# Optimization experiments

Measured on AMD Instinct MI355X. Metric: run time of the kernel, lower is better.

The kernel has to match this reference:

```python
import jax, jax.numpy as jnp
import numpy as np

T, B, IN, H1, H2, H3 = 128, 256, 512, 1024, 1024, 512


def _glorot(key, shape, fan):
    bound = 1.0 / np.sqrt(fan)
    return jax.random.uniform(key, shape, jnp.float32, -bound, bound)


def _cell_params(key, in_dim, h_dim):
    k = jax.random.split(key, 4)
    return (_glorot(k[0], (4 * h_dim, in_dim), h_dim),
            _glorot(k[1], (4 * h_dim, h_dim), h_dim),
            _glorot(k[2], (4 * h_dim,), h_dim),
            _glorot(k[3], (4 * h_dim,), h_dim))


def setup_inputs() -> dict:
    key = jax.random.key(0)
    ks = jax.random.split(key, 4)
    x = jax.random.normal(ks[0], (T, B, IN), jnp.float32)
    Wih1, Whh1, bih1, bhh1 = _cell_params(ks[1], IN, H1)
    Wih2, Whh2, bih2, bhh2 = _cell_params(ks[2], H1, H2)
    Wih3, Whh3, bih3, bhh3 = _cell_params(ks[3], H2, H3)
    return dict(input_seq=x,
                Wih1=Wih1, Whh1=Whh1, bih1=bih1, bhh1=bhh1,
                Wih2=Wih2, Whh2=Whh2, bih2=bih2, bhh2=bhh2,
                Wih3=Wih3, Whh3=Whh3, bih3=bih3, bhh3=bhh3)


def _lstm_cell(x, h, c, Wih, Whh, bih, bhh):
    # PyTorch LSTMCell gate order: i, f, g, o
    gates = x @ Wih.T + bih + h @ Whh.T + bhh
    i, f, g, o = jnp.split(gates, 4, axis=-1)
    c_new = jax.nn.sigmoid(f) * c + jax.nn.sigmoid(i) * jnp.tanh(g)
    h_new = jax.nn.sigmoid(o) * jnp.tanh(c_new)
    return h_new, c_new


def reference(input_seq, Wih1, Whh1, bih1, bhh1,
              Wih2, Whh2, bih2, bhh2,
              Wih3, Whh3, bih3, bhh3):
    Bn = input_seq.shape[1]
    init = (jnp.zeros((Bn, H1)), jnp.zeros((Bn, H1)),
            jnp.zeros((Bn, H2)), jnp.zeros((Bn, H2)),
            jnp.zeros((Bn, H3)), jnp.zeros((Bn, H3)))

    def step(carry, x_t):
        h1, c1, h2, c2, h3, c3 = carry
        h1, c1 = _lstm_cell(x_t, h1, c1, Wih1, Whh1, bih1, bhh1)
        h2, c2 = _lstm_cell(h1, h2, c2, Wih2, Whh2, bih2, bhh2)
        h3, c3 = _lstm_cell(h2, h3, c3, Wih3, Whh3, bih3, bhh3)
        return (h1, c1, h2, c2, h3, c3), None

    final, _ = jax.lax.scan(step, init, input_seq)
    return final
```

## Files before the change

### kernel.cpp

```cpp
#include <hip/hip_runtime.h>
#include <hip/hip_bf16.h>
#include <cstdint>
#include <cstddef>


typedef __attribute__((ext_vector_type(8))) short short8;
typedef __attribute__((ext_vector_type(4))) short short4v;
typedef __attribute__((ext_vector_type(4))) float floatx4;

#define NBLK 256
#define NTHR 1024

__device__ __forceinline__ float fsig(float x) {
    x = fminf(fmaxf(x, -30.f), 30.f);
    return 1.f / (1.f + __expf(-x));
}
__device__ __forceinline__ float ftanh(float x) {
    x = fminf(fmaxf(x, -15.f), 15.f);
    float e = __expf(2.f * x);
    return (e - 1.f) / (e + 1.f);
}

__device__ __forceinline__ int get_xcc() {
    int x;
    asm volatile("s_getreg_b32 %0, hwreg(HW_REG_XCC_ID)" : "=s"(x));
    return x & 7;
}


__device__ __forceinline__ void safe_sync(int* sy) {
    __syncthreads();
    if (threadIdx.x == 0) {
        int a = __hip_atomic_fetch_add(sy + 704, 1, __ATOMIC_ACQ_REL, __HIP_MEMORY_SCOPE_AGENT);
        if (a == NBLK - 1)
            __hip_atomic_store(sy + 768, 1, __ATOMIC_RELEASE, __HIP_MEMORY_SCOPE_AGENT);
        while (__hip_atomic_load(sy + 768, __ATOMIC_RELAXED, __HIP_MEMORY_SCOPE_AGENT) == 0)
            __builtin_amdgcn_s_sleep(2);
        __builtin_amdgcn_fence(__ATOMIC_ACQUIRE, "agent");
    }
    __syncthreads();
}

__device__ __forceinline__ void grid_sync(int* sy, int myx, int myM, int G,
                                          int myr, int round) {
    __syncthreads();
    if (threadIdx.x == 0) {
        int* gen = sy + 576;
        int g = __hip_atomic_load(gen, __ATOMIC_RELAXED, __HIP_MEMORY_SCOPE_AGENT);
        int a = __hip_atomic_fetch_add(sy + myx * 64, 1, __ATOMIC_RELAXED, __HIP_MEMORY_SCOPE_AGENT);
        if ((a + 1) % myM == 0) {
            int m = __hip_atomic_fetch_add(sy + 512, 1, __ATOMIC_RELAXED, __HIP_MEMORY_SCOPE_AGENT);
            if ((m + 1) % G == 0)
                __hip_atomic_fetch_add(gen, 1, __ATOMIC_RELAXED, __HIP_MEMORY_SCOPE_AGENT);
        }
        while (__hip_atomic_load(gen, __ATOMIC_RELAXED, __HIP_MEMORY_SCOPE_AGENT) == g)
            __builtin_amdgcn_s_sleep(2);
        int* ep = sy + 832 + myx * 16;
        if (myr == 0) {
            __builtin_amdgcn_fence(__ATOMIC_ACQUIRE, "agent");
            __hip_atomic_store(ep, round, __ATOMIC_RELEASE, __HIP_MEMORY_SCOPE_AGENT);
        } else {
            while (__hip_atomic_load(ep, __ATOMIC_RELAXED, __HIP_MEMORY_SCOPE_AGENT) < round)
                __builtin_amdgcn_s_sleep(1);
            asm volatile("buffer_inv sc0\n\ts_waitcnt vmcnt(0)" ::: "memory");
        }
    }
    __syncthreads();
}

template<int K1, int K2, int H>
__global__ void pack_frag_kernel(const float* __restrict__ Wih,
                                 const float* __restrict__ Whh,
                                 __hip_bfloat16* __restrict__ dst) {
    constexpr int NK = (K1 + K2) / 32;
    constexpr int NTT = H / 4;
    int idx = blockIdx.x * 256 + threadIdx.x;
    if (idx >= NTT * NK * 64) return;
    int slot = idx & 63;
    int kc = (idx >> 6) % NK;
    int b = idx / (64 * NK);
    int du = slot & 3, g = (slot >> 2) & 3, ksub = slot >> 4;
    int unit = b * 4 + du;
    int j = g * H + unit;
    int k0 = kc * 32 + ksub * 8;
    __hip_bfloat16 tmp[8];
#pragma unroll
    for (int e = 0; e < 8; ++e) {
        int k = k0 + e;
        float v = (k < K1) ? Wih[(size_t)j * K1 + k] : Whh[(size_t)j * K2 + (k - K1)];
        tmp[e] = __float2bfloat16(v);
    }
    *(short8*)(dst + (size_t)idx * 8) = *(short8*)tmp;
}

__global__ void pack_bias_kernel(const float* __restrict__ a,
                                 const float* __restrict__ b,
                                 int n, float* __restrict__ out) {
    int i = blockIdx.x * 256 + threadIdx.x;
    if (i < n) out[i] = a[i] + b[i];
}

__global__ void x_to_slab_kernel(const float* __restrict__ x,
                                 __hip_bfloat16* __restrict__ xs) {
    int idx = blockIdx.x * 256 + threadIdx.x;
    int j   = idx & 7;
    int row = (idx >> 3) & 255;
    int s   = (idx >> 11) & 63;
    int t   = idx >> 17;
    xs[idx] = __float2bfloat16(x[((size_t)(t * 256 + row)) * 512 + s * 8 + j]);
}

__global__ void zero_f32_kernel(float* p, int n) {
    int i = blockIdx.x * 256 + threadIdx.x;
    if (i < n) p[i] = 0.f;
}

__global__ void zero_i32_kernel(int* p, int n) {
    int i = blockIdx.x * 256 + threadIdx.x;
    if (i < n) p[i] = 0;
}

__device__ __forceinline__ short8 afrag8(const __hip_bfloat16* __restrict__ base, int k) {
    return *(const short8*)(base + (size_t)k * 8192);
}
__device__ __forceinline__ short8 afrag4(const __hip_bfloat16* __restrict__ base, int k) {
    const __hip_bfloat16* p = base + (size_t)k * 8192;
    short4v lo = *(const short4v*)p;
    short4v hi = *(const short4v*)(p + 1024);
    return (short8){lo.x, lo.y, lo.z, lo.w, hi.x, hi.y, hi.z, hi.w};
}

template<int NK1, int NK2, bool A2W4, int NT, int H, int TSTR>
__device__ __forceinline__ void run_layer(
    const short8* __restrict__ ldsw, int bslot0,
    const __hip_bfloat16* __restrict__ A1, const __hip_bfloat16* __restrict__ A2,
    const float (&bl)[NT],
    __hip_bfloat16* __restrict__ hs, int slab,
    float (&creg)[NT][4], int tbase, int lane, int wave,
    bool fin, float* __restrict__ ho, float* __restrict__ co)
{
    constexpr int NK = NK1 + NK2;
    constexpr int W = NT * 4;
    const int col = lane & 15, ksub = lane >> 4;
    const int row = wave * 16 + col;
    const __hip_bfloat16* __restrict__ a1 = A1 + ksub * 2048 + row * 8;
    const __hip_bfloat16* __restrict__ a2 = A2 + ksub * 2048 + (A2W4 ? row * 4 : row * 8);

    short8 rb[4];
#pragma unroll
    for (int i = 0; i < 4; ++i) rb[i] = afrag8(a1, i);

    floatx4 acc[NT];
#pragma unroll
    for (int ti = 0; ti < NT; ++ti) acc[ti] = (floatx4){0.f, 0.f, 0.f, 0.f};

#pragma unroll 4
    for (int kc = 0; kc < NK; ++kc) {
#pragma unroll
        for (int ti = 0; ti < NT; ++ti)
            acc[ti] = __builtin_amdgcn_mfma_f32_16x16x32_bf16(
                rb[kc & 3], ldsw[bslot0 + ti * TSTR + kc * 64], acc[ti], 0, 0, 0);
        int kn = kc + 4;
        if (kn < NK)
            rb[kc & 3] = (kn < NK1) ? afrag8(a1, kn)
                        : (A2W4 ? afrag4(a2, kn - NK1) : afrag8(a2, kn - NK1));
    }

    const int du = col & 3;
    const int sbase = ksub * 16 + du;
#pragma unroll
    for (int ti = 0; ti < NT; ++ti) {
        float avb[4];
#pragma unroll
        for (int r = 0; r < 4; ++r) avb[r] = acc[ti][r] + bl[ti];
#pragma unroll
        for (int r = 0; r < 4; ++r) {
            float gI = __shfl(avb[r], sbase);
            float gF = __shfl(avb[r], sbase + 4);
            float gG = __shfl(avb[r], sbase + 8);
            float gO = __shfl(avb[r], sbase + 12);
            float i_ = fsig(gI), f_ = fsig(gF), gg = ftanh(gG), o_ = fsig(gO);
            float cn = f_ * creg[ti][r] + i_ * gg;
            creg[ti][r] = cn;
            float hn = o_ * ftanh(cn);
            __hip_bfloat16 hv = __float2bfloat16(hn);
            unsigned hb = (unsigned)*reinterpret_cast<unsigned short*>(&hv);
            unsigned hp = __shfl(hb, lane + 1);
            int orow = wave * 16 + ksub * 4 + r;
            if (col < 4) {
                if ((col & 1) == 0) {
                    unsigned pk = hb | (hp << 16);
                    size_t idx = ((size_t)slab * 256 + orow) * W + ti * 4 + col;
                    __hip_atomic_store((unsigned*)(hs + idx), pk,
                                       __ATOMIC_RELAXED, __HIP_MEMORY_SCOPE_AGENT);
                }
                if (fin) {
                    int unit = (tbase + ti) * 4 + du;
                    ho[(size_t)orow * H + unit] = hn;
                    co[(size_t)orow * H + unit] = cn;
                }
            }
        }
    }
}

__global__ __launch_bounds__(NTHR, 4) void lstm_persistent(
    const __hip_bfloat16* __restrict__ xs,
    const __hip_bfloat16* __restrict__ w1f,
    const __hip_bfloat16* __restrict__ w2f,
    const __hip_bfloat16* __restrict__ w3f,
    const float* __restrict__ bc1, const float* __restrict__ bc2, const float* __restrict__ bc3,
    __hip_bfloat16* __restrict__ h1b, __hip_bfloat16* __restrict__ h2b,
    __hip_bfloat16* __restrict__ h3b,
    float* __restrict__ out, int* syncp)
{
    __shared__ short8 ldsw[9216];
    __shared__ int smeta[4];
    const int tid = threadIdx.x, blk = blockIdx.x;
    const int lane = tid & 63, wave = tid >> 6;
    const bool isA = blk < 128;
    const int sb = isA ? blk : (blk - 128);

    if (isA) {
        const short8* s2 = (const short8*)w2f + (size_t)sb * 8192;
        for (int i = tid; i < 8192; i += NTHR) ldsw[i] = s2[i];
    } else {
        const short8* s1 = (const short8*)w1f + (size_t)sb * 6144;
        for (int i = tid; i < 6144; i += NTHR) ldsw[i] = s1[i];
        const short8* s3 = (const short8*)w3f + (size_t)sb * 3072;
        for (int i = tid; i < 3072; i += NTHR) ldsw[6144 + i] = s3[i];
    }

    int myx = 0, myM = 1, G = 1;
    if (tid == 0) {
        myx = get_xcc();
        int r = __hip_atomic_fetch_add(syncp + 640 + myx, 1, __ATOMIC_RELAXED, __HIP_MEMORY_SCOPE_AGENT);
        smeta[0] = myx;
        smeta[2] = r;
    }
    safe_sync(syncp);
    if (tid == 0) {
        myM = __hip_atomic_load(syncp + 640 + myx, __ATOMIC_RELAXED, __HIP_MEMORY_SCOPE_AGENT);
        G = 0;
        for (int x = 0; x < 8; ++x)
            G += (__hip_atomic_load(syncp + 640 + x, __ATOMIC_RELAXED, __HIP_MEMORY_SCOPE_AGENT) > 0);
        if (myM < 1) myM = 1;
        if (G < 1) G = 1;
        smeta[1] = myM;
    }
    __syncthreads();
    const int myx_a = smeta[0];
    const int myM_a = smeta[1];
    const int myr_a = smeta[2];

    const int col = lane & 15, ksub = lane >> 4, du = col & 3, g = col >> 2;
    (void)ksub; (void)col;

    float bl1[2], bl2[2], bl3[1];
    if (isA) {
        bl2[0] = bc2[g * 1024 + (2 * sb + 0) * 4 + du];
        bl2[1] = bc2[g * 1024 + (2 * sb + 1) * 4 + du];
        bl1[0] = bl1[1] = bl3[0] = 0.f;
    } else {
        bl1[0] = bc1[g * 1024 + (2 * sb + 0) * 4 + du];
        bl1[1] = bc1[g * 1024 + (2 * sb + 1) * 4 + du];
        bl3[0] = bc3[g * 512 + sb * 4 + du];
        bl2[0] = bl2[1] = 0.f;
    }

    float c1r[2][4] = {{0.f,0.f,0.f,0.f},{0.f,0.f,0.f,0.f}};
    float c2r[2][4] = {{0.f,0.f,0.f,0.f},{0.f,0.f,0.f,0.f}};
    float c3r[1][4] = {{0.f,0.f,0.f,0.f}};

    float* h1o = out;
    float* c1o = out + 262144;
    float* h2o = out + 524288;
    float* c2o = out + 786432;
    float* h3o = out + 1048576;
    float* c3o = out + 1179648;

    if (!isA) {
        run_layer<16, 32, false, 2, 1024, 3072>(ldsw, lane,
            xs, h1b + 262144, bl1, h1b, sb, c1r, 2 * sb, lane, wave, false, h1o, c1o);
    }
    grid_sync(syncp, myx_a, myM_a, G, myr_a, 1);

    for (int t = 0; t < 128; ++t) {
        const size_t cur = (size_t)(t & 1), prv = (size_t)((t + 1) & 1);
        if (isA) {
            run_layer<32, 32, false, 2, 1024, 4096>(ldsw, lane,
                h1b + cur * 262144, h2b + prv * 262144, bl2,
                h2b + cur * 262144, sb, c2r, 2 * sb, lane, wave, t == 127, h2o, c2o);
        } else {
            if (t < 127) {
                run_layer<16, 32, false, 2, 1024, 3072>(ldsw, lane,
                    xs + (size_t)(t + 1) * 131072, h1b + cur * 262144, bl1,
                    h1b + prv * 262144, sb, c1r, 2 * sb, lane, wave, (t + 1) == 127, h1o, c1o);
            }
            if (t >= 1) {
                run_layer<32, 16, true, 1, 512, 0>(ldsw, 6144 + lane,
                    h2b + prv * 262144, h3b + cur * 131072, bl3,
                    h3b + prv * 131072, sb, c3r, sb, lane, wave, false, h3o, c3o);
            }
        }
        grid_sync(syncp, myx_a, myM_a, G, myr_a, t + 2);
    }

    if (!isA) {
        run_layer<32, 16, true, 1, 512, 0>(ldsw, 6144 + lane,
            h2b + 262144, h3b, bl3, h3b + 131072, sb, c3r, sb, lane, wave, true, h3o, c3o);
    }
}

extern "C" void kernel_launch(void* const* d_in, const int* in_sizes, int n_in,
                              void* d_out, int out_size, void* d_ws, size_t ws_size,
                              hipStream_t stream) {
    const float* x    = (const float*)d_in[0];
    const float* Wih1 = (const float*)d_in[1];
    const float* Whh1 = (const float*)d_in[2];
    const float* bih1 = (const float*)d_in[3];
    const float* bhh1 = (const float*)d_in[4];
    const float* Wih2 = (const float*)d_in[5];
    const float* Whh2 = (const float*)d_in[6];
    const float* bih2 = (const float*)d_in[7];
    const float* bhh2 = (const float*)d_in[8];
    const float* Wih3 = (const float*)d_in[9];
    const float* Whh3 = (const float*)d_in[10];
    const float* bih3 = (const float*)d_in[11];
    const float* bhh3 = (const float*)d_in[12];
    float* out = (float*)d_out;

    char* p = (char*)d_ws;
    auto alloc = [&](size_t bytes) {
        char* r = p;
        p += (bytes + 255) & ~(size_t)255;
        return r;
    };
    __hip_bfloat16* xs  = (__hip_bfloat16*)alloc((size_t)128 * 64 * 256 * 8 * 2);
    __hip_bfloat16* w1f = (__hip_bfloat16*)alloc((size_t)256 * 48 * 64 * 8 * 2);
    __hip_bfloat16* w2f = (__hip_bfloat16*)alloc((size_t)256 * 64 * 64 * 8 * 2);
    __hip_bfloat16* w3f = (__hip_bfloat16*)alloc((size_t)128 * 48 * 64 * 8 * 2);
    float* bc1 = (float*)alloc(4096 * 4);
    float* bc2 = (float*)alloc(4096 * 4);
    float* bc3 = (float*)alloc(2048 * 4);
    __hip_bfloat16* h1b = (__hip_bfloat16*)alloc((size_t)2 * 262144 * 2);
    __hip_bfloat16* h2b = (__hip_bfloat16*)alloc((size_t)2 * 262144 * 2);
    __hip_bfloat16* h3b = (__hip_bfloat16*)alloc((size_t)2 * 131072 * 2);
    int* syncp = (int*)alloc(4096);

    auto blocks = [](int n) { return (n + 255) / 256; };

    pack_frag_kernel<512, 1024, 1024><<<blocks(256 * 48 * 64), 256, 0, stream>>>(Wih1, Whh1, w1f);
    pack_frag_kernel<1024, 1024, 1024><<<blocks(256 * 64 * 64), 256, 0, stream>>>(Wih2, Whh2, w2f);
    pack_frag_kernel<1024, 512, 512><<<blocks(128 * 48 * 64), 256, 0, stream>>>(Wih3, Whh3, w3f);
    pack_bias_kernel<<<blocks(4096), 256, 0, stream>>>(bih1, bhh1, 4096, bc1);
    pack_bias_kernel<<<blocks(4096), 256, 0, stream>>>(bih2, bhh2, 4096, bc2);
    pack_bias_kernel<<<blocks(2048), 256, 0, stream>>>(bih3, bhh3, 2048, bc3);
    x_to_slab_kernel<<<blocks(128 * 256 * 512), 256, 0, stream>>>(x, xs);
    zero_f32_kernel<<<blocks(262144), 256, 0, stream>>>((float*)h1b, 262144);
    zero_f32_kernel<<<blocks(262144), 256, 0, stream>>>((float*)h2b, 262144);
    zero_f32_kernel<<<blocks(131072), 256, 0, stream>>>((float*)h3b, 131072);
    zero_i32_kernel<<<1, 1024, 0, stream>>>(syncp, 1024);

    lstm_persistent<<<NBLK, NTHR, 0, stream>>>(xs, w1f, w2f, w3f, bc1, bc2, bc3,
                                               h1b, h2b, h3b, out, syncp);
}
```

Before: 3.833 ms.

## Remap waves to two row tiles per column tile to share LDS weight fragments

Each wave now computes two 16-row batch tiles for a single column tile, instead of one row tile for two column tiles. The LDS weight fragment is read once and fed to two MFMAs, which halves LDS weight traffic per MFMA but doubles the global activation fragment loads per wave. Layer 3, which has only one column tile, now runs on only half the waves (wave < 8), which may leave that phase underutilised. The G value is also now passed through shared memory so all threads use the same value.

```diff
diff --git a/kernel.cpp b/kernel.cpp
--- a/kernel.cpp
+++ b/kernel.cpp
@@ -130,49 +130,57 @@
     return (short8){lo.x, lo.y, lo.z, lo.w, hi.x, hi.y, hi.z, hi.w};
 }
 
-template<int NK1, int NK2, bool A2W4, int NT, int H, int TSTR>
+template<int NK1, int NK2, bool A2W4, int NCT, int H>
 __device__ __forceinline__ void run_layer(
     const short8* __restrict__ ldsw, int bslot0,
     const __hip_bfloat16* __restrict__ A1, const __hip_bfloat16* __restrict__ A2,
-    const float (&bl)[NT],
+    float bl,
     __hip_bfloat16* __restrict__ hs, int slab,
-    float (&creg)[NT][4], int tbase, int lane, int wave,
+    float (&creg)[2][4], int tbase, int lane, int wave, int myti,
     bool fin, float* __restrict__ ho, float* __restrict__ co)
 {
     constexpr int NK = NK1 + NK2;
-    constexpr int W = NT * 4;
+    constexpr int W = NCT * 4;
     const int col = lane & 15, ksub = lane >> 4;
-    const int row = wave * 16 + col;
-    const __hip_bfloat16* __restrict__ a1 = A1 + ksub * 2048 + row * 8;
-    const __hip_bfloat16* __restrict__ a2 = A2 + ksub * 2048 + (A2W4 ? row * 4 : row * 8);
-
-    short8 rb[4];
-#pragma unroll
-    for (int i = 0; i < 4; ++i) rb[i] = afrag8(a1, i);
-
-    floatx4 acc[NT];
-#pragma unroll
-    for (int ti = 0; ti < NT; ++ti) acc[ti] = (floatx4){0.f, 0.f, 0.f, 0.f};
+    const int rg = wave & 7;
+    const int r0 = rg * 32 + col;
+    const __hip_bfloat16* __restrict__ a1_0 = A1 + ksub * 2048 + r0 * 8;
+    const __hip_bfloat16* __restrict__ a1_1 = a1_0 + 16 * 8;
+    const __hip_bfloat16* __restrict__ a2_0 = A2 + ksub * 2048 + (A2W4 ? r0 * 4 : r0 * 8);
+    const __hip_bfloat16* __restrict__ a2_1 = a2_0 + (A2W4 ? 16 * 4 : 16 * 8);
+
+    short8 rb0[4], rb1[4];
+#pragma unroll
+    for (int i = 0; i < 4; ++i) {
+        rb0[i] = afrag8(a1_0, i);
+        rb1[i] = afrag8(a1_1, i);
+    }
+
+    floatx4 acc0 = (floatx4){0.f, 0.f, 0.f, 0.f};
+    floatx4 acc1 = (floatx4){0.f, 0.f, 0.f, 0.f};
 
 #pragma unroll 4
     for (int kc = 0; kc < NK; ++kc) {
-#pragma unroll
-        for (int ti = 0; ti < NT; ++ti)
-            acc[ti] = __builtin_amdgcn_mfma_f32_16x16x32_bf16(
-                rb[kc & 3], ldsw[bslot0 + ti * TSTR + kc * 64], acc[ti], 0, 0, 0);
+        short8 b = ldsw[bslot0 + kc * 64];
+        acc0 = __builtin_amdgcn_mfma_f32_16x16x32_bf16(rb0[kc & 3], b, acc0, 0, 0, 0);
+        acc1 = __builtin_amdgcn_mfma_f32_16x16x32_bf16(rb1[kc & 3], b, acc1, 0, 0, 0);
         int kn = kc + 4;
-        if (kn < NK)
-            rb[kc & 3] = (kn < NK1) ? afrag8(a1, kn)
-                        : (A2W4 ? afrag4(a2, kn - NK1) : afrag8(a2, kn - NK1));
+        if (kn < NK) {
+            rb0[kc & 3] = (kn < NK1) ? afrag8(a1_0, kn)
+                         : (A2W4 ? afrag4(a2_0, kn - NK1) : afrag8(a2_0, kn - NK1));
+            rb1[kc & 3] = (kn < NK1) ? afrag8(a1_1, kn)
+                         : (A2W4 ? afrag4(a2_1, kn - NK1) : afrag8(a2_1, kn - NK1));
+        }
     }
 
     const int du = col & 3;
     const int sbase = ksub * 16 + du;
 #pragma unroll
-    for (int ti = 0; ti < NT; ++ti) {
+    for (int rt = 0; rt < 2; ++rt) {
+        const floatx4 acc = rt ? acc1 : acc0;
         float avb[4];
 #pragma unroll
-        for (int r = 0; r < 4; ++r) avb[r] = acc[ti][r] + bl[ti];
+        for (int r = 0; r < 4; ++r) avb[r] = acc[r] + bl;
 #pragma unroll
         for (int r = 0; r < 4; ++r) {
             float gI = __shfl(avb[r], sbase);
@@ -180,22 +188,22 @@
             float gG = __shfl(avb[r], sbase + 8);
             float gO = __shfl(avb[r], sbase + 12);
             float i_ = fsig(gI), f_ = fsig(gF), gg = ftanh(gG), o_ = fsig(gO);
-            float cn = f_ * creg[ti][r] + i_ * gg;
-            creg[ti][r] = cn;
+            float cn = f_ * creg[rt][r] + i_ * gg;
+            creg[rt][r] = cn;
             float hn = o_ * ftanh(cn);
             __hip_bfloat16 hv = __float2bfloat16(hn);
             unsigned hb = (unsigned)*reinterpret_cast<unsigned short*>(&hv);
             unsigned hp = __shfl(hb, lane + 1);
-            int orow = wave * 16 + ksub * 4 + r;
+            int orow = rg * 32 + rt * 16 + ksub * 4 + r;
             if (col < 4) {
                 if ((col & 1) == 0) {
                     unsigned pk = hb | (hp << 16);
-                    size_t idx = ((size_t)slab * 256 + orow) * W + ti * 4 + col;
+                    size_t idx = ((size_t)slab * 256 + orow) * W + myti * 4 + col;
                     __hip_atomic_store((unsigned*)(hs + idx), pk,
                                        __ATOMIC_RELAXED, __HIP_MEMORY_SCOPE_AGENT);
                 }
                 if (fin) {
-                    int unit = (tbase + ti) * 4 + du;
+                    int unit = (tbase + myti) * 4 + du;
                     ho[(size_t)orow * H + unit] = hn;
                     co[(size_t)orow * H + unit] = cn;
                 }
@@ -231,46 +239,44 @@
         for (int i = tid; i < 3072; i += NTHR) ldsw[6144 + i] = s3[i];
     }
 
-    int myx = 0, myM = 1, G = 1;
     if (tid == 0) {
-        myx = get_xcc();
+        int myx = get_xcc();
         int r = __hip_atomic_fetch_add(syncp + 640 + myx, 1, __ATOMIC_RELAXED, __HIP_MEMORY_SCOPE_AGENT);
         smeta[0] = myx;
         smeta[2] = r;
     }
     safe_sync(syncp);
     if (tid == 0) {
-        myM = __hip_atomic_load(syncp + 640 + myx, __ATOMIC_RELAXED, __HIP_MEMORY_SCOPE_AGENT);
-        G = 0;
+        int myx = smeta[0];
+        int m = __hip_atomic_load(syncp + 640 + myx, __ATOMIC_RELAXED, __HIP_MEMORY_SCOPE_AGENT);
+        int G = 0;
         for (int x = 0; x < 8; ++x)
             G += (__hip_atomic_load(syncp + 640 + x, __ATOMIC_RELAXED, __HIP_MEMORY_SCOPE_AGENT) > 0);
-        if (myM < 1) myM = 1;
+        if (m < 1) m = 1;
         if (G < 1) G = 1;
-        smeta[1] = myM;
+        smeta[1] = m;
+        smeta[3] = G;
     }
     __syncthreads();
     const int myx_a = smeta[0];
     const int myM_a = smeta[1];
     const int myr_a = smeta[2];
-
-    const int col = lane & 15, ksub = lane >> 4, du = col & 3, g = col >> 2;
-    (void)ksub; (void)col;
-
-    float bl1[2], bl2[2], bl3[1];
+    const int G_a   = smeta[3];
+
+    const int col = lane & 15, du = col & 3, g = col >> 2;
+    const int myti = wave >> 3;
+
+    float bl1 = 0.f, bl2 = 0.f, bl3 = 0.f;
     if (isA) {
-        bl2[0] = bc2[g * 1024 + (2 * sb + 0) * 4 + du];
-        bl2[1] = bc2[g * 1024 + (2 * sb + 1) * 4 + du];
-        bl1[0] = bl1[1] = bl3[0] = 0.f;
+        bl2 = bc2[g * 1024 + (2 * sb + myti) * 4 + du];
     } else {
-        bl1[0] = bc1[g * 1024 + (2 * sb + 0) * 4 + du];
-        bl1[1] = bc1[g * 1024 + (2 * sb + 1) * 4 + du];
-        bl3[0] = bc3[g * 512 + sb * 4 + du];
-        bl2[0] = bl2[1] = 0.f;
+        bl1 = bc1[g * 1024 + (2 * sb + myti) * 4 + du];
+        bl3 = bc3[g * 512 + sb * 4 + du];
     }
 
     float c1r[2][4] = {{0.f,0.f,0.f,0.f},{0.f,0.f,0.f,0.f}};
     float c2r[2][4] = {{0.f,0.f,0.f,0.f},{0.f,0.f,0.f,0.f}};
-    float c3r[1][4] = {{0.f,0.f,0.f,0.f}};
+    float c3r[2][4] = {{0.f,0.f,0.f,0.f},{0.f,0.f,0.f,0.f}};
 
     float* h1o = out;
     float* c1o = out + 262144;
@@ -280,35 +286,40 @@
     float* c3o = out + 1179648;
 
     if (!isA) {
-        run_layer<16, 32, false, 2, 1024, 3072>(ldsw, lane,
-            xs, h1b + 262144, bl1, h1b, sb, c1r, 2 * sb, lane, wave, false, h1o, c1o);
-    }
-    grid_sync(syncp, myx_a, myM_a, G, myr_a, 1);
+        run_layer<16, 32, false, 2, 1024>(ldsw, lane + myti * 3072,
+            xs, h1b + 262144, bl1, h1b, sb, c1r, 2 * sb, lane, wave, myti,
+            false, h1o, c1o);
+    }
+    grid_sync(syncp, myx_a, myM_a, G_a, myr_a, 1);
 
     for (int t = 0; t < 128; ++t) {
         const size_t cur = (size_t)(t & 1), prv = (size_t)((t + 1) & 1);
         if (isA) {
-            run_layer<32, 32, false, 2, 1024, 4096>(ldsw, lane,
+            run_layer<32, 32, false, 2, 1024>(ldsw, lane + myti * 4096,
                 h1b + cur * 262144, h2b + prv * 262144, bl2,
-                h2b + cur * 262144, sb, c2r, 2 * sb, lane, wave, t == 127, h2o, c2o);
+                h2b + cur * 262144, sb, c2r, 2 * sb, lane, wave, myti,
+                t == 127, h2o, c2o);
         } else {
             if (t < 127) {
-                run_layer<16, 32, false, 2, 1024, 3072>(ldsw, lane,
+                run_layer<16, 32, false, 2, 1024>(ldsw, lane + myti * 3072,
                     xs + (size_t)(t + 1) * 131072, h1b + cur * 262144, bl1,
-                    h1b + prv * 262144, sb, c1r, 2 * sb, lane, wave, (t + 1) == 127, h1o, c1o);
+                    h1b + prv * 262144, sb, c1r, 2 * sb, lane, wave, myti,
+                    (t + 1) == 127, h1o, c1o);
             }
-            if (t >= 1) {
-                run_layer<32, 16, true, 1, 512, 0>(ldsw, 6144 + lane,
+            if (t >= 1 && wave < 8) {
+                run_layer<32, 16, true, 1, 512>(ldsw, 6144 + lane,
                     h2b + prv * 262144, h3b + cur * 131072, bl3,
-                    h3b + prv * 131072, sb, c3r, sb, lane, wave, false, h3o, c3o);
+                    h3b + prv * 131072, sb, c3r, sb, lane, wave, 0,
+                    false, h3o, c3o);
             }
         }
-        grid_sync(syncp, myx_a, myM_a, G, myr_a, t + 2);
-    }
-
-    if (!isA) {
-        run_layer<32, 16, true, 1, 512, 0>(ldsw, 6144 + lane,
-            h2b + 262144, h3b, bl3, h3b + 131072, sb, c3r, sb, lane, wave, true, h3o, c3o);
+        grid_sync(syncp, myx_a, myM_a, G_a, myr_a, t + 2);
+    }
+
+    if (!isA && wave < 8) {
+        run_layer<32, 16, true, 1, 512>(ldsw, 6144 + lane,
+            h2b + 262144, h3b, bl3, h3b + 131072, sb, c3r, sb, lane, wave, 0,
+            true, h3o, c3o);
     }
 }
 
```

Result: slower. 4.843 ms (+26.3%).

## Replace per-step grid barrier with per-layer dataflow counters and 8-deep state ring

Applied to the files above, without the earlier changes.

Each timestep's full grid barrier is replaced by per-step, per-layer completion counters. Blocks wait only on the specific hidden-state producers they depend on and then invalidate L1. The hidden-state buffers become an 8-slot ring so producers can run ahead, with a full grid barrier kept every 4 steps to bound that lead. This is meant to remove barrier stalls and let layers pipeline more loosely, at the cost of extra atomics and spin-waits per layer step.

```diff
diff --git a/kernel.cpp b/kernel.cpp
--- a/kernel.cpp
+++ b/kernel.cpp
@@ -25,6 +25,19 @@
     int x;
     asm volatile("s_getreg_b32 %0, hwreg(HW_REG_XCC_ID)" : "=s"(x));
     return x & 7;
+}
+
+__device__ __forceinline__ void l1_inv() {
+    asm volatile("buffer_inv sc0\n\ts_waitcnt vmcnt(0)" ::: "memory");
+}
+
+__device__ __forceinline__ void wait_cnt(int* c, int target) {
+    while (__hip_atomic_load(c, __ATOMIC_RELAXED, __HIP_MEMORY_SCOPE_AGENT) < target)
+        __builtin_amdgcn_s_sleep(1);
+}
+
+__device__ __forceinline__ void signal_cnt(int* c) {
+    __hip_atomic_fetch_add(c, 1, __ATOMIC_RELAXED, __HIP_MEMORY_SCOPE_AGENT);
 }
 
 
@@ -62,7 +75,7 @@
         } else {
             while (__hip_atomic_load(ep, __ATOMIC_RELAXED, __HIP_MEMORY_SCOPE_AGENT) < round)
                 __builtin_amdgcn_s_sleep(1);
-            asm volatile("buffer_inv sc0\n\ts_waitcnt vmcnt(0)" ::: "memory");
+            l1_inv();
         }
     }
     __syncthreads();
@@ -210,8 +223,8 @@
     const __hip_bfloat16* __restrict__ w2f,
     const __hip_bfloat16* __restrict__ w3f,
     const float* __restrict__ bc1, const float* __restrict__ bc2, const float* __restrict__ bc3,
-    __hip_bfloat16* __restrict__ h1b, __hip_bfloat16* __restrict__ h2b,
-    __hip_bfloat16* __restrict__ h3b,
+    __hip_bfloat16* __restrict__ h1a, __hip_bfloat16* __restrict__ h2a,
+    __hip_bfloat16* __restrict__ h3a,
     float* __restrict__ out, int* syncp)
 {
     __shared__ short8 ldsw[9216];
@@ -231,30 +244,39 @@
         for (int i = tid; i < 3072; i += NTHR) ldsw[6144 + i] = s3[i];
     }
 
-    int myx = 0, myM = 1, G = 1;
     if (tid == 0) {
-        myx = get_xcc();
+        int myx = get_xcc();
         int r = __hip_atomic_fetch_add(syncp + 640 + myx, 1, __ATOMIC_RELAXED, __HIP_MEMORY_SCOPE_AGENT);
         smeta[0] = myx;
         smeta[2] = r;
     }
     safe_sync(syncp);
     if (tid == 0) {
-        myM = __hip_atomic_load(syncp + 640 + myx, __ATOMIC_RELAXED, __HIP_MEMORY_SCOPE_AGENT);
-        G = 0;
+        int myx = smeta[0];
+        int m = __hip_atomic_load(syncp + 640 + myx, __ATOMIC_RELAXED, __HIP_MEMORY_SCOPE_AGENT);
+        int G = 0;
         for (int x = 0; x < 8; ++x)
             G += (__hip_atomic_load(syncp + 640 + x, __ATOMIC_RELAXED, __HIP_MEMORY_SCOPE_AGENT) > 0);
-        if (myM < 1) myM = 1;
+        if (m < 1) m = 1;
         if (G < 1) G = 1;
-        smeta[1] = myM;
+        smeta[1] = m;
+        smeta[3] = G;
     }
     __syncthreads();
     const int myx_a = smeta[0];
     const int myM_a = smeta[1];
     const int myr_a = smeta[2];
-
-    const int col = lane & 15, ksub = lane >> 4, du = col & 3, g = col >> 2;
-    (void)ksub; (void)col;
+    const int G_a   = smeta[3];
+
+    int* d1 = syncp + 1024;
+    int* d2 = syncp + 1280;
+    int* d3 = syncp + 1536;
+
+    auto H1S = [&](int s) { return h1a + (size_t)((s + 16) & 7) * 262144; };
+    auto H2S = [&](int s) { return h2a + (size_t)((s + 16) & 7) * 262144; };
+    auto H3S = [&](int s) { return h3a + (size_t)((s + 16) & 7) * 131072; };
+
+    const int col = lane & 15, du = col & 3, g = col >> 2;
 
     float bl1[2], bl2[2], bl3[1];
     if (isA) {
@@ -281,34 +303,63 @@
 
     if (!isA) {
         run_layer<16, 32, false, 2, 1024, 3072>(ldsw, lane,
-            xs, h1b + 262144, bl1, h1b, sb, c1r, 2 * sb, lane, wave, false, h1o, c1o);
-    }
-    grid_sync(syncp, myx_a, myM_a, G, myr_a, 1);
-
+            xs, H1S(-1), bl1, H1S(0), sb, c1r, 2 * sb, lane, wave, false, h1o, c1o);
+        __syncthreads();
+        if (tid == 0) signal_cnt(d1 + 0);
+    }
+
+    int rnd = 1;
     for (int t = 0; t < 128; ++t) {
-        const size_t cur = (size_t)(t & 1), prv = (size_t)((t + 1) & 1);
+        if ((t & 3) == 0)
+            grid_sync(syncp, myx_a, myM_a, G_a, myr_a, rnd++);
+
         if (isA) {
+            if (tid == 0) {
+                wait_cnt(d1 + t, 128);
+                if (t >= 1) wait_cnt(d2 + t - 1, 128);
+                l1_inv();
+            }
+            __syncthreads();
             run_layer<32, 32, false, 2, 1024, 4096>(ldsw, lane,
-                h1b + cur * 262144, h2b + prv * 262144, bl2,
-                h2b + cur * 262144, sb, c2r, 2 * sb, lane, wave, t == 127, h2o, c2o);
+                H1S(t), H2S(t - 1), bl2,
+                H2S(t), sb, c2r, 2 * sb, lane, wave, t == 127, h2o, c2o);
+            __syncthreads();
+            if (tid == 0) signal_cnt(d2 + t);
         } else {
             if (t < 127) {
+                if (tid == 0) { wait_cnt(d1 + t, 128); l1_inv(); }
+                __syncthreads();
                 run_layer<16, 32, false, 2, 1024, 3072>(ldsw, lane,
-                    xs + (size_t)(t + 1) * 131072, h1b + cur * 262144, bl1,
-                    h1b + prv * 262144, sb, c1r, 2 * sb, lane, wave, (t + 1) == 127, h1o, c1o);
+                    xs + (size_t)(t + 1) * 131072, H1S(t), bl1,
+                    H1S(t + 1), sb, c1r, 2 * sb, lane, wave, (t + 1) == 127, h1o, c1o);
+                __syncthreads();
+                if (tid == 0) signal_cnt(d1 + t + 1);
             }
             if (t >= 1) {
+                if (tid == 0) {
+                    wait_cnt(d2 + t - 1, 128);
+                    if (t >= 2) wait_cnt(d3 + t - 2, 128);
+                    l1_inv();
+                }
+                __syncthreads();
                 run_layer<32, 16, true, 1, 512, 0>(ldsw, 6144 + lane,
-                    h2b + prv * 262144, h3b + cur * 131072, bl3,
-                    h3b + prv * 131072, sb, c3r, sb, lane, wave, false, h3o, c3o);
+                    H2S(t - 1), H3S(t - 2), bl3,
+                    H3S(t - 1), sb, c3r, sb, lane, wave, false, h3o, c3o);
+                __syncthreads();
+                if (tid == 0) signal_cnt(d3 + t - 1);
             }
         }
-        grid_sync(syncp, myx_a, myM_a, G, myr_a, t + 2);
     }
 
     if (!isA) {
+        if (tid == 0) {
+            wait_cnt(d2 + 127, 128);
+            wait_cnt(d3 + 126, 128);
+            l1_inv();
+        }
+        __syncthreads();
         run_layer<32, 16, true, 1, 512, 0>(ldsw, 6144 + lane,
-            h2b + 262144, h3b, bl3, h3b + 131072, sb, c3r, sb, lane, wave, true, h3o, c3o);
+            H2S(127), H3S(126), bl3, H3S(127), sb, c3r, sb, lane, wave, true, h3o, c3o);
     }
 }
 
@@ -343,10 +394,10 @@
     float* bc1 = (float*)alloc(4096 * 4);
     float* bc2 = (float*)alloc(4096 * 4);
     float* bc3 = (float*)alloc(2048 * 4);
-    __hip_bfloat16* h1b = (__hip_bfloat16*)alloc((size_t)2 * 262144 * 2);
-    __hip_bfloat16* h2b = (__hip_bfloat16*)alloc((size_t)2 * 262144 * 2);
-    __hip_bfloat16* h3b = (__hip_bfloat16*)alloc((size_t)2 * 131072 * 2);
-    int* syncp = (int*)alloc(4096);
+    __hip_bfloat16* h1a = (__hip_bfloat16*)alloc((size_t)8 * 262144 * 2);
+    __hip_bfloat16* h2a = (__hip_bfloat16*)alloc((size_t)8 * 262144 * 2);
+    __hip_bfloat16* h3a = (__hip_bfloat16*)alloc((size_t)8 * 131072 * 2);
+    int* syncp = (int*)alloc(32768);
 
     auto blocks = [](int n) { return (n + 255) / 256; };
 
@@ -357,11 +408,11 @@
     pack_bias_kernel<<<blocks(4096), 256, 0, stream>>>(bih2, bhh2, 4096, bc2);
     pack_bias_kernel<<<blocks(2048), 256, 0, stream>>>(bih3, bhh3, 2048, bc3);
     x_to_slab_kernel<<<blocks(128 * 256 * 512), 256, 0, stream>>>(x, xs);
-    zero_f32_kernel<<<blocks(262144), 256, 0, stream>>>((float*)h1b, 262144);
-    zero_f32_kernel<<<blocks(262144), 256, 0, stream>>>((float*)h2b, 262144);
-    zero_f32_kernel<<<blocks(131072), 256, 0, stream>>>((float*)h3b, 131072);
-    zero_i32_kernel<<<1, 1024, 0, stream>>>(syncp, 1024);
+    zero_f32_kernel<<<blocks(1048576), 256, 0, stream>>>((float*)h1a, 1048576);
+    zero_f32_kernel<<<blocks(1048576), 256, 0, stream>>>((float*)h2a, 1048576);
+    zero_f32_kernel<<<blocks(524288), 256, 0, stream>>>((float*)h3a, 524288);
+    zero_i32_kernel<<<blocks(8192), 256, 0, stream>>>(syncp, 8192);
 
     lstm_persistent<<<NBLK, NTHR, 0, stream>>>(xs, w1f, w2f, w3f, bc1, bc2, bc3,
-                                               h1b, h2b, h3b, out, syncp);
-}
+                                               h1a, h2a, h3a, out, syncp);
+}
```

New measurement: 3.619 ms. 1.06x faster.
